# Kernel tuning notes

Measured on AMD Instinct MI355X. Metric: run time of the kernel, lower is better.

The kernel has to match this reference:

```python
import jax, jax.numpy as jnp
import numpy as np


def setup_inputs() -> dict:
    key = jax.random.key(0)
    k1, k2, k3, k4 = jax.random.split(key, 4)
    B, C, H, Wd = 32, 512, 32, 32
    sparse_dim, dict_size, feature_dim = 1024, 1024, 512
    x = jax.random.normal(k1, (B, C, H, Wd), dtype=jnp.float32)
    dictionary = jax.random.normal(k2, (dict_size, feature_dim), dtype=jnp.float32)
    # scale W, S like the LISTA init (|| . || ~ O(1)) so iterates stay bounded
    W = jax.random.normal(k3, (sparse_dim, feature_dim), dtype=jnp.float32) * 0.02
    S = jax.random.normal(k4, (sparse_dim, sparse_dim), dtype=jnp.float32) * 0.02
    thresh = jnp.float32(0.1)
    return {"x": x, "dictionary": dictionary, "W": W, "S": S, "thresh": thresh, "num_steps": 5}


def _soft_threshold(z, thresh):
    return jnp.sign(z) * jnp.maximum(jnp.abs(z) - thresh, 0.0)


def reference(x, dictionary, W, S, thresh, num_steps):
    B, C, H, Wd = x.shape
    sparse_dim = S.shape[0]
    # [B,C,H,W] -> [B*H*W, C]
    x_flat = jnp.transpose(x, (0, 2, 3, 1)).reshape(-1, C)
    dict_norm = dictionary / jnp.linalg.norm(dictionary, axis=1, keepdims=True)
    # W @ x^T is loop-invariant; compute once. [K, N]
    Wx = W @ x_flat.T
    z = jnp.zeros((sparse_dim, x_flat.shape[0]), dtype=x.dtype)
    for _ in range(num_steps):
        z = z + Wx
        z = z - S @ z
        z = _soft_threshold(z, thresh)
    # [K,N] -> [B,K,H,W]
    z = jnp.transpose(z.T.reshape(B, H, Wd, sparse_dim), (0, 3, 1, 2))
    return (z, dict_norm)
```

## Files before the change

### kernel.cpp

```cpp
#include <hip/hip_runtime.h>
#include <hip/hip_bf16.h>

typedef __bf16 bf16_t;
typedef __bf16 bf16x4 __attribute__((ext_vector_type(4)));
typedef __bf16 bf16x8 __attribute__((ext_vector_type(8)));
typedef float f32x4 __attribute__((ext_vector_type(4)));

#define GLOAD_LDS16(g, l)                                                      \
  __builtin_amdgcn_global_load_lds(                                            \
      (const __attribute__((address_space(1))) void*)(g),                      \
      (__attribute__((address_space(3))) void*)(l), 16, 0, 0)

#define MFMA(a, b, c) __builtin_amdgcn_mfma_f32_16x16x32_bf16((a), (b), (c), 0, 0, 0)

__global__ __launch_bounds__(512, 2) void gemm_kernel(
    const bf16_t* __restrict__ A, const bf16_t* __restrict__ Bt,
    int Kd, int Nc, int mode,
    const bf16_t* __restrict__ WxIn, bf16_t* __restrict__ UnextOrWx,
    float* __restrict__ Out, const float* __restrict__ thresh_p)
{
  __shared__ __align__(16) char smem[147456];
  bf16_t* lds = (bf16_t*)smem;

  const int tid = threadIdx.x;
  const int wid = tid >> 6, lane = tid & 63;
  const int wr = wid >> 1, wc = wid & 1;
  const int lr = lane & 15, kg = lane >> 4;

  const int per = gridDim.x >> 3;
  const int logical = (blockIdx.x & 7) * per + (blockIdx.x >> 3);
  const int ntn = Nc >> 7;
  const int tileN = (logical % ntn) << 7;
  const int tileM = (logical / ntn) << 8;
  const int NT = Kd >> 6;

  size_t offA[4]; int dstA[4];
  #pragma unroll
  for (int j = 0; j < 4; ++j) {
    const int f = j * 512 + tid;
    const int row = f >> 3, u = f & 7;
    const int ug = u ^ (row & 7);
    offA[j] = (size_t)(tileM + row) * Kd + ug * 8;
    dstA[j] = f * 8;
  }
  size_t offB[2]; int dstB[2];
  #pragma unroll
  for (int j = 0; j < 2; ++j) {
    const int f = j * 512 + tid;
    const int col = f >> 3, u = f & 7;
    const int ug = u ^ (col & 7);
    offB[j] = (size_t)(tileN + col) * Kd + ug * 8;
    dstB[j] = 16384 + f * 8;
  }

  auto readA = [&](int mi, int ks, int bs) -> bf16x8 {
    const int R = wr * 64 + mi * 16 + lr;
    const int ul = (ks * 4 + kg) ^ (R & 7);
    return *(const bf16x8*)(lds + bs + R * 64 + ul * 8);
  };
  auto readB = [&](int ni, int ks, int bs) -> bf16x8 {
    const int C = wc * 64 + ni * 16 + lr;
    const int ul = (ks * 4 + kg) ^ (C & 7);
    return *(const bf16x8*)(lds + bs + 16384 + C * 64 + ul * 8);
  };

  f32x4 acc[4][4] = {};
  bf16x8 a0[4], b0[4], a1[4], b1[4];

  #pragma unroll
  for (int j = 0; j < 4; ++j) GLOAD_LDS16(A + offA[j], lds + dstA[j]);
  #pragma unroll
  for (int j = 0; j < 2; ++j) GLOAD_LDS16(Bt + offB[j], lds + dstB[j]);
  if (NT > 1) {
    #pragma unroll
    for (int j = 0; j < 4; ++j) GLOAD_LDS16(A + offA[j] + 64, lds + 24576 + dstA[j]);
    #pragma unroll
    for (int j = 0; j < 2; ++j) GLOAD_LDS16(Bt + offB[j] + 64, lds + 24576 + dstB[j]);
  }
  asm volatile("s_waitcnt vmcnt(6)" ::: "memory");
  __builtin_amdgcn_s_barrier();

  int buf = 0, sb3 = 2;
  for (int t = 0; t < NT; ++t) {
    const int bs = buf * 24576;
    const int sbs = sb3 * 24576;
    const int ts = (t + 2 < NT) ? t + 2 : t + 2 - NT;
    const size_t ko = (size_t)ts << 6;

    GLOAD_LDS16(A + offA[0] + ko, lds + sbs + dstA[0]);
    GLOAD_LDS16(A + offA[1] + ko, lds + sbs + dstA[1]);
    GLOAD_LDS16(A + offA[2] + ko, lds + sbs + dstA[2]);
    GLOAD_LDS16(A + offA[3] + ko, lds + sbs + dstA[3]);
    GLOAD_LDS16(Bt + offB[0] + ko, lds + sbs + dstB[0]);
    GLOAD_LDS16(Bt + offB[1] + ko, lds + sbs + dstB[1]);

    #pragma unroll
    for (int mi = 0; mi < 4; ++mi) a0[mi] = readA(mi, 0, bs);
    #pragma unroll
    for (int ni = 0; ni < 4; ++ni) b0[ni] = readB(ni, 0, bs);
    #pragma unroll
    for (int mi = 0; mi < 4; ++mi) a1[mi] = readA(mi, 1, bs);
    #pragma unroll
    for (int ni = 0; ni < 4; ++ni) b1[ni] = readB(ni, 1, bs);

    #pragma unroll
    for (int mi = 0; mi < 4; ++mi)
      #pragma unroll
      for (int ni = 0; ni < 4; ++ni)
        acc[mi][ni] = MFMA(a0[mi], b0[ni], acc[mi][ni]);
    #pragma unroll
    for (int mi = 0; mi < 4; ++mi)
      #pragma unroll
      for (int ni = 0; ni < 4; ++ni)
        acc[mi][ni] = MFMA(a1[mi], b1[ni], acc[mi][ni]);

    asm volatile("s_waitcnt vmcnt(6)" ::: "memory");
    __builtin_amdgcn_s_barrier();

    buf = (buf == 2) ? 0 : buf + 1;
    sb3 = (sb3 == 2) ? 0 : sb3 + 1;
  }

  const float th = *thresh_p;

  if (mode <= 1) {
    asm volatile("s_waitcnt vmcnt(0)" ::: "memory");
    __syncthreads();
    float* Tl = (float*)smem;
    #pragma unroll
    for (int c = 0; c < 8; ++c) {
      if (c) __syncthreads();
      if (wr == (c >> 1)) {
        #pragma unroll
        for (int mj = 0; mj < 2; ++mj) {
          const int mi = (c & 1) * 2 + mj;
          const int rl = mj * 16 + kg * 4;
          #pragma unroll
          for (int ni = 0; ni < 4; ++ni) {
            const int cl = wc * 64 + ni * 16 + lr;
            #pragma unroll
            for (int r = 0; r < 4; ++r)
              Tl[(rl + r) * 132 + cl] = acc[mi][ni][r];
          }
        }
      }
      __syncthreads();
      #pragma unroll
      for (int j = 0; j < 2; ++j) {
        const int f  = j * 512 + tid;
        const int rl = f >> 5;
        const int c4 = (f & 31) * 4;
        const f32x4 v = *(const f32x4*)&Tl[rl * 132 + c4];
        const int grow = tileM + c * 32 + rl;
        const size_t gidx = (size_t)grow * Nc + tileN + c4;
        bf16x4 ov;
        if (mode == 1) {
          const bf16x4 wx = *(const bf16x4*)&WxIn[gidx];
          #pragma unroll
          for (int e = 0; e < 4; ++e) {
            const float a  = fabsf(v[e]) - th;
            const float zn = (a > 0.f) ? copysignf(a, v[e]) : 0.f;
            ov[e] = (bf16_t)(zn + (float)wx[e]);
          }
        } else {
          #pragma unroll
          for (int e = 0; e < 4; ++e) ov[e] = (bf16_t)v[e];
        }
        *(bf16x4*)&UnextOrWx[gidx] = ov;
      }
    }
  } else {
    #pragma unroll
    for (int mi = 0; mi < 4; ++mi)
      #pragma unroll
      for (int ni = 0; ni < 4; ++ni)
        #pragma unroll
        for (int r = 0; r < 4; ++r) {
          const float v = acc[mi][ni][r];
          const float a = fabsf(v) - th;
          acc[mi][ni][r] = (a > 0.f) ? copysignf(a, v) : 0.f;
        }
    asm volatile("s_waitcnt vmcnt(0)" ::: "memory");
    __syncthreads();
    float* Tl = (float*)smem;
    const int    bb    = tileM >> 10;
    const size_t obase = (size_t)bb * 1048576 + (size_t)(tileM & 1023);
    #pragma unroll
    for (int ch = 0; ch < 4; ++ch) {
      if (ch) __syncthreads();
      if (wc == (ch >> 1)) {
        #pragma unroll
        for (int nj = 0; nj < 2; ++nj) {
          const int ni = (ch & 1) * 2 + nj;
          const int cp = nj * 16 + lr;
          #pragma unroll
          for (int mi = 0; mi < 4; ++mi)
            #pragma unroll
            for (int r = 0; r < 4; ++r)
              Tl[cp * 260 + wr * 64 + mi * 16 + kg * 4 + r] = acc[mi][ni][r];
        }
      }
      __syncthreads();
      #pragma unroll
      for (int j = 0; j < 4; ++j) {
        const int f  = j * 512 + tid;
        const int cp = f >> 6;
        const int p4 = (f & 63) * 4;
        const f32x4 v = *(const f32x4*)&Tl[cp * 260 + p4];
        *(f32x4*)&Out[obase + (size_t)(tileN + ch * 32 + cp) * 1024 + p4] = v;
      }
    }
  }
}

__global__ __launch_bounds__(512, 2) void gemm_dual_kernel(
    const bf16_t* __restrict__ A, const bf16_t* __restrict__ B1,
    const bf16_t* __restrict__ B2,
    bf16_t* __restrict__ WxOut, bf16_t* __restrict__ UOut,
    const float* __restrict__ thresh_p)
{
  __shared__ __align__(16) char smem[131072];
  bf16_t* lds = (bf16_t*)smem;

  const int tid = threadIdx.x;
  const int wid = tid >> 6, lane = tid & 63;
  const int wr = wid >> 1, wc = wid & 1;
  const int lr = lane & 15, kg = lane >> 4;

  const int per = gridDim.x >> 3;
  const int logical = (blockIdx.x & 7) * per + (blockIdx.x >> 3);
  const int tileN = (logical & 7) << 7;
  const int tileM = (logical >> 3) << 8;

  size_t offA[4]; int dstA[4];
  #pragma unroll
  for (int j = 0; j < 4; ++j) {
    const int f = j * 512 + tid;
    const int row = f >> 3, u = f & 7;
    const int ug = u ^ (row & 7);
    offA[j] = (size_t)(tileM + row) * 512 + ug * 8;
    dstA[j] = f * 8;
  }
  size_t offB[2]; int dstB1[2], dstB2[2];
  #pragma unroll
  for (int j = 0; j < 2; ++j) {
    const int f = j * 512 + tid;
    const int col = f >> 3, u = f & 7;
    const int ug = u ^ (col & 7);
    offB[j] = (size_t)(tileN + col) * 512 + ug * 8;
    dstB1[j] = 16384 + f * 8;
    dstB2[j] = 24576 + f * 8;
  }

  auto readA = [&](int mi, int ks, int bs) -> bf16x8 {
    const int R = wr * 64 + mi * 16 + lr;
    const int ul = (ks * 4 + kg) ^ (R & 7);
    return *(const bf16x8*)(lds + bs + R * 64 + ul * 8);
  };
  auto readB = [&](int boff, int ni, int ks, int bs) -> bf16x8 {
    const int C = wc * 64 + ni * 16 + lr;
    const int ul = (ks * 4 + kg) ^ (C & 7);
    return *(const bf16x8*)(lds + bs + boff + C * 64 + ul * 8);
  };

  f32x4 accW[4][4] = {}, accT[4][4] = {};
  bf16x8 af[4], bw[4], bt[4];

  auto stageTile = [&](int ts, int sbs) {
    const size_t ko = (size_t)ts << 6;
    #pragma unroll
    for (int j = 0; j < 4; ++j) GLOAD_LDS16(A + offA[j] + ko, lds + sbs + dstA[j]);
    #pragma unroll
    for (int j = 0; j < 2; ++j) GLOAD_LDS16(B1 + offB[j] + ko, lds + sbs + dstB1[j]);
    #pragma unroll
    for (int j = 0; j < 2; ++j) GLOAD_LDS16(B2 + offB[j] + ko, lds + sbs + dstB2[j]);
  };

  stageTile(0, 0);
  asm volatile("s_waitcnt vmcnt(0)" ::: "memory");
  __builtin_amdgcn_s_barrier();

  for (int t = 0; t < 8; ++t) {
    const int bs  = (t & 1) << 15;
    const int sbs = bs ^ 32768;
    stageTile((t + 1 < 8) ? t + 1 : 0, sbs);

    #pragma unroll
    for (int ks = 0; ks < 2; ++ks) {
      #pragma unroll
      for (int mi = 0; mi < 4; ++mi) af[mi] = readA(mi, ks, bs);
      #pragma unroll
      for (int ni = 0; ni < 4; ++ni) bw[ni] = readB(16384, ni, ks, bs);
      #pragma unroll
      for (int ni = 0; ni < 4; ++ni) bt[ni] = readB(24576, ni, ks, bs);
      #pragma unroll
      for (int mi = 0; mi < 4; ++mi)
        #pragma unroll
        for (int ni = 0; ni < 4; ++ni) {
          accW[mi][ni] = MFMA(af[mi], bw[ni], accW[mi][ni]);
          accT[mi][ni] = MFMA(af[mi], bt[ni], accT[mi][ni]);
        }
    }

    asm volatile("s_waitcnt vmcnt(0)" ::: "memory");
    __builtin_amdgcn_s_barrier();
  }

  const float th = *thresh_p;
  asm volatile("s_waitcnt vmcnt(0)" ::: "memory");
  __syncthreads();
  float* Tl = (float*)smem;

  #pragma unroll
  for (int c = 0; c < 8; ++c) {
    if (c) __syncthreads();
    if (wr == (c >> 1)) {
      #pragma unroll
      for (int mj = 0; mj < 2; ++mj) {
        const int mi = (c & 1) * 2 + mj;
        const int rl = mj * 16 + kg * 4;
        #pragma unroll
        for (int ni = 0; ni < 4; ++ni) {
          const int cl = wc * 64 + ni * 16 + lr;
          #pragma unroll
          for (int r = 0; r < 4; ++r)
            Tl[(rl + r) * 132 + cl] = accW[mi][ni][r];
        }
      }
    }
    __syncthreads();
    f32x4 vw[2];
    #pragma unroll
    for (int j = 0; j < 2; ++j) {
      const int f  = j * 512 + tid;
      const int rl = f >> 5;
      const int c4 = (f & 31) * 4;
      vw[j] = *(const f32x4*)&Tl[rl * 132 + c4];
      const int grow = tileM + c * 32 + rl;
      const size_t gidx = (size_t)grow * 1024 + tileN + c4;
      bf16x4 ov;
      #pragma unroll
      for (int e = 0; e < 4; ++e) ov[e] = (bf16_t)vw[j][e];
      *(bf16x4*)&WxOut[gidx] = ov;
    }
    __syncthreads();
    if (wr == (c >> 1)) {
      #pragma unroll
      for (int mj = 0; mj < 2; ++mj) {
        const int mi = (c & 1) * 2 + mj;
        const int rl = mj * 16 + kg * 4;
        #pragma unroll
        for (int ni = 0; ni < 4; ++ni) {
          const int cl = wc * 64 + ni * 16 + lr;
          #pragma unroll
          for (int r = 0; r < 4; ++r)
            Tl[(rl + r) * 132 + cl] = accT[mi][ni][r];
        }
      }
    }
    __syncthreads();
    #pragma unroll
    for (int j = 0; j < 2; ++j) {
      const int f  = j * 512 + tid;
      const int rl = f >> 5;
      const int c4 = (f & 31) * 4;
      const f32x4 vt = *(const f32x4*)&Tl[rl * 132 + c4];
      const int grow = tileM + c * 32 + rl;
      const size_t gidx = (size_t)grow * 1024 + tileN + c4;
      bf16x4 ov;
      #pragma unroll
      for (int e = 0; e < 4; ++e) {
        const float a  = fabsf(vt[e]) - th;
        const float zn = (a > 0.f) ? copysignf(a, vt[e]) : 0.f;
        ov[e] = (bf16_t)(zn + vw[j][e]);
      }
      *(bf16x4*)&UOut[gidx] = ov;
    }
  }
}

__global__ __launch_bounds__(256) void tw_gemm_kernel(
    const bf16_t* __restrict__ Tb,
    const bf16_t* __restrict__ Wt,
    bf16_t* __restrict__ TW)
{
  const int tid = threadIdx.x;
  const int wid = tid >> 6, lane = tid & 63;
  const int lr = lane & 15, kg = lane >> 4;
  const int tile = blockIdx.x * 4 + wid;
  const int ci = tile & 31;
  const int ii = tile >> 5;
  const int i0 = ii * 16, c0 = ci * 16;

  const bf16_t* pa = Tb + (size_t)(i0 + lr) * 1024 + kg * 8;
  const bf16_t* pb = Wt + (size_t)(c0 + lr) * 1024 + kg * 8;

  f32x4 acc = {};
  #pragma unroll 4
  for (int t = 0; t < 32; ++t) {
    const bf16x8 a = *(const bf16x8*)(pa + t * 32);
    const bf16x8 b = *(const bf16x8*)(pb + t * 32);
    acc = MFMA(a, b, acc);
  }
  #pragma unroll
  for (int r = 0; r < 4; ++r)
    TW[(size_t)(i0 + kg * 4 + r) * 512 + c0 + lr] = (bf16_t)acc[r];
}

__global__ void make_T_castW_kernel(const float* __restrict__ S,
                                    bf16_t* __restrict__ T,
                                    const float* __restrict__ W,
                                    bf16_t* __restrict__ Wb) {
  const int idx = blockIdx.x * blockDim.x + threadIdx.x;
  const int i = idx >> 10, j = idx & 1023;
  T[idx] = (bf16_t)(((i == j) ? 1.0f : 0.0f) - S[idx]);
  if (idx < 524288) Wb[idx] = (bf16_t)W[idx];
}

__global__ void transpose_cast_x_kernel(const float* __restrict__ x,
                                        bf16_t* __restrict__ xt) {
  __shared__ float t[32][33];
  const int b  = blockIdx.z;
  const int p0 = blockIdx.x * 32;
  const int c0 = blockIdx.y * 32;
  const int tx = threadIdx.x, ty = threadIdx.y;
  #pragma unroll
  for (int i = 0; i < 32; i += 8)
    t[ty + i][tx] = x[((size_t)b * 512 + c0 + ty + i) * 1024 + p0 + tx];
  __syncthreads();
  #pragma unroll
  for (int i = 0; i < 32; i += 8)
    xt[((size_t)b * 1024 + p0 + ty + i) * 512 + c0 + tx] = (bf16_t)t[tx][ty + i];
}

__global__ void transpose_cast_w_kernel(const float* __restrict__ W,
                                        bf16_t* __restrict__ Wt) {
  __shared__ float t[32][33];
  const int j0 = blockIdx.x * 32;
  const int c0 = blockIdx.y * 32;
  const int tx = threadIdx.x, ty = threadIdx.y;
  #pragma unroll
  for (int i = 0; i < 32; i += 8)
    t[ty + i][tx] = W[(size_t)(j0 + ty + i) * 512 + c0 + tx];
  __syncthreads();
  #pragma unroll
  for (int i = 0; i < 32; i += 8)
    Wt[(size_t)(c0 + ty + i) * 1024 + j0 + tx] = (bf16_t)t[tx][ty + i];
}

__global__ void dict_norm_kernel(const float* __restrict__ dict,
                                 float* __restrict__ out) {
  const int row = blockIdx.x;
  const int tid = threadIdx.x;
  const float* r = dict + (size_t)row * 512;
  float s = 0.f;
  for (int i = tid; i < 512; i += 256) { float v = r[i]; s += v * v; }
  #pragma unroll
  for (int off = 32; off > 0; off >>= 1) s += __shfl_down(s, off);
  __shared__ float ps[4];
  if ((tid & 63) == 0) ps[tid >> 6] = s;
  __syncthreads();
  const float inv = 1.0f / sqrtf(ps[0] + ps[1] + ps[2] + ps[3]);
  for (int i = tid; i < 512; i += 256) out[(size_t)row * 512 + i] = r[i] * inv;
}

extern "C" void kernel_launch(void* const* d_in, const int* in_sizes, int n_in,
                              void* d_out, int out_size, void* d_ws, size_t ws_size,
                              hipStream_t stream) {
  const float* x      = (const float*)d_in[0];
  const float* dict   = (const float*)d_in[1];
  const float* W      = (const float*)d_in[2];
  const float* S      = (const float*)d_in[3];
  const float* thresh = (const float*)d_in[4];

  float* out = (float*)d_out;

  char* ws = (char*)d_ws;
  bf16_t* uA   = (bf16_t*)ws;
  bf16_t* uB   = (bf16_t*)(ws + 67108864);
  bf16_t* WxBf = (bf16_t*)(ws + 134217728);
  bf16_t* xt   = (bf16_t*)(ws + 201326592);
  bf16_t* Wbf  = (bf16_t*)(ws + 234881024);
  bf16_t* Tbf  = (bf16_t*)(ws + 235929600);

  bf16_t* WtBf = (bf16_t*)out;
  bf16_t* TWbf = WtBf + 524288;
  float* dnorm = out + 33554432;

  make_T_castW_kernel<<<dim3(2048), dim3(512), 0, stream>>>(S, Tbf, W, Wbf);
  transpose_cast_w_kernel<<<dim3(32, 16), dim3(32, 8), 0, stream>>>(W, WtBf);
  tw_gemm_kernel<<<dim3(512), dim3(256), 0, stream>>>(Tbf, WtBf, TWbf);
  transpose_cast_x_kernel<<<dim3(32, 16, 32), dim3(32, 8), 0, stream>>>(x, xt);
  dict_norm_kernel<<<dim3(1024), dim3(256), 0, stream>>>(dict, dnorm);

  gemm_dual_kernel<<<dim3(1024), dim3(512), 0, stream>>>(
      xt, Wbf, TWbf, WxBf, uA, thresh);

  bf16_t* uc = uA; bf16_t* un = uB;
  for (int s = 0; s < 3; ++s) {
    gemm_kernel<<<dim3(1024), dim3(512), 0, stream>>>(
        uc, Tbf, 1024, 1024, 1, WxBf, un, nullptr, thresh);
    bf16_t* tmp = uc; uc = un; un = tmp;
  }
  gemm_kernel<<<dim3(1024), dim3(512), 0, stream>>>(
      uc, Tbf, 1024, 1024, 2, nullptr, nullptr, out, thresh);
}
```

Measured before the change: 504.9 us.

## Load B operand directly from global into registers, staging only A in LDS

Operand B is no longer staged in LDS. Each wave loads its B fragments straight from global memory into registers, double-buffered one k-tile ahead, while A keeps the 3-stage LDS pipeline. This cuts LDS traffic and footprint (147KB to 98KB) and removes the B LDS reads. The cost is redundant global loads of B across the waves that share a column, plus more registers. The wait count was raised to account for the extra outstanding loads, which looks fragile, and the unroll by two assumes NT is even.

```diff
diff --git a/kernel.cpp b/kernel.cpp
--- a/kernel.cpp
+++ b/kernel.cpp
@@ -19,7 +19,7 @@
     const bf16_t* __restrict__ WxIn, bf16_t* __restrict__ UnextOrWx,
     float* __restrict__ Out, const float* __restrict__ thresh_p)
 {
-  __shared__ __align__(16) char smem[147456];
+  __shared__ __align__(16) char smem[98304];
   bf16_t* lds = (bf16_t*)smem;
 
   const int tid = threadIdx.x;
@@ -43,82 +43,78 @@
     offA[j] = (size_t)(tileM + row) * Kd + ug * 8;
     dstA[j] = f * 8;
   }
-  size_t offB[2]; int dstB[2];
-  #pragma unroll
-  for (int j = 0; j < 2; ++j) {
-    const int f = j * 512 + tid;
-    const int col = f >> 3, u = f & 7;
-    const int ug = u ^ (col & 7);
-    offB[j] = (size_t)(tileN + col) * Kd + ug * 8;
-    dstB[j] = 16384 + f * 8;
-  }
+
+  const bf16_t* baseB = Bt + (size_t)(tileN + wc * 64 + lr) * Kd + kg * 8;
+  const size_t strideB16 = (size_t)16 * Kd;
 
   auto readA = [&](int mi, int ks, int bs) -> bf16x8 {
     const int R = wr * 64 + mi * 16 + lr;
     const int ul = (ks * 4 + kg) ^ (R & 7);
     return *(const bf16x8*)(lds + bs + R * 64 + ul * 8);
   };
-  auto readB = [&](int ni, int ks, int bs) -> bf16x8 {
-    const int C = wc * 64 + ni * 16 + lr;
-    const int ul = (ks * 4 + kg) ^ (C & 7);
-    return *(const bf16x8*)(lds + bs + 16384 + C * 64 + ul * 8);
-  };
 
   f32x4 acc[4][4] = {};
-  bf16x8 a0[4], b0[4], a1[4], b1[4];
-
-  #pragma unroll
-  for (int j = 0; j < 4; ++j) GLOAD_LDS16(A + offA[j], lds + dstA[j]);
-  #pragma unroll
-  for (int j = 0; j < 2; ++j) GLOAD_LDS16(Bt + offB[j], lds + dstB[j]);
-  if (NT > 1) {
-    #pragma unroll
-    for (int j = 0; j < 4; ++j) GLOAD_LDS16(A + offA[j] + 64, lds + 24576 + dstA[j]);
-    #pragma unroll
-    for (int j = 0; j < 2; ++j) GLOAD_LDS16(Bt + offB[j] + 64, lds + 24576 + dstB[j]);
-  }
-  asm volatile("s_waitcnt vmcnt(6)" ::: "memory");
-  __builtin_amdgcn_s_barrier();
+  bf16x8 a0[4], a1[4];
+  bf16x8 bA[8], bB[8];
 
   int buf = 0, sb3 = 2;
-  for (int t = 0; t < NT; ++t) {
-    const int bs = buf * 24576;
-    const int sbs = sb3 * 24576;
+
+  auto iter = [&](int t, bf16x8 (&bc)[8], bf16x8 (&bn)[8]) {
+    const int bs = buf * 16384;
+    const int sbs = sb3 * 16384;
+    const int tb = (t + 1 < NT) ? t + 1 : 0;
     const int ts = (t + 2 < NT) ? t + 2 : t + 2 - NT;
+    const size_t kb = (size_t)tb << 6;
     const size_t ko = (size_t)ts << 6;
 
+    #pragma unroll
+    for (int ni = 0; ni < 4; ++ni) {
+      bn[ni]     = *(const bf16x8*)(baseB + ni * strideB16 + kb);
+      bn[ni + 4] = *(const bf16x8*)(baseB + ni * strideB16 + kb + 32);
+    }
     GLOAD_LDS16(A + offA[0] + ko, lds + sbs + dstA[0]);
     GLOAD_LDS16(A + offA[1] + ko, lds + sbs + dstA[1]);
     GLOAD_LDS16(A + offA[2] + ko, lds + sbs + dstA[2]);
     GLOAD_LDS16(A + offA[3] + ko, lds + sbs + dstA[3]);
-    GLOAD_LDS16(Bt + offB[0] + ko, lds + sbs + dstB[0]);
-    GLOAD_LDS16(Bt + offB[1] + ko, lds + sbs + dstB[1]);
 
     #pragma unroll
     for (int mi = 0; mi < 4; ++mi) a0[mi] = readA(mi, 0, bs);
     #pragma unroll
-    for (int ni = 0; ni < 4; ++ni) b0[ni] = readB(ni, 0, bs);
-    #pragma unroll
     for (int mi = 0; mi < 4; ++mi) a1[mi] = readA(mi, 1, bs);
-    #pragma unroll
-    for (int ni = 0; ni < 4; ++ni) b1[ni] = readB(ni, 1, bs);
 
     #pragma unroll
     for (int mi = 0; mi < 4; ++mi)
       #pragma unroll
       for (int ni = 0; ni < 4; ++ni)
-        acc[mi][ni] = MFMA(a0[mi], b0[ni], acc[mi][ni]);
+        acc[mi][ni] = MFMA(a0[mi], bc[ni], acc[mi][ni]);
     #pragma unroll
     for (int mi = 0; mi < 4; ++mi)
       #pragma unroll
       for (int ni = 0; ni < 4; ++ni)
-        acc[mi][ni] = MFMA(a1[mi], b1[ni], acc[mi][ni]);
-
-    asm volatile("s_waitcnt vmcnt(6)" ::: "memory");
+        acc[mi][ni] = MFMA(a1[mi], bc[ni + 4], acc[mi][ni]);
+
+    asm volatile("s_waitcnt vmcnt(12)" ::: "memory");
     __builtin_amdgcn_s_barrier();
 
     buf = (buf == 2) ? 0 : buf + 1;
     sb3 = (sb3 == 2) ? 0 : sb3 + 1;
+  };
+
+  #pragma unroll
+  for (int j = 0; j < 4; ++j) GLOAD_LDS16(A + offA[j], lds + dstA[j]);
+  #pragma unroll
+  for (int j = 0; j < 4; ++j) GLOAD_LDS16(A + offA[j] + 64, lds + 16384 + dstA[j]);
+  #pragma unroll
+  for (int ni = 0; ni < 4; ++ni) {
+    bA[ni]     = *(const bf16x8*)(baseB + ni * strideB16);
+    bA[ni + 4] = *(const bf16x8*)(baseB + ni * strideB16 + 32);
+  }
+  asm volatile("s_waitcnt vmcnt(12)" ::: "memory");
+  __builtin_amdgcn_s_barrier();
+
+  for (int t = 0; t < NT; t += 2) {
+    iter(t,     bA, bB);
+    iter(t + 1, bB, bA);
   }
 
   const float th = *thresh_p;
```

Result: slower. 862.6 us (+70.9%).

## Use 256x256 tiles with 8-wave phased ping-pong pipeline in iteration GEMMs

Applied to the files above, without the earlier changes.

Replaces the 256x128 triple-buffered GEMM with a 256x256 tile kernel (8 waves in a 2x4 grid, 128x64 per wave) and a double-buffered LDS schedule. Each K-step is split into four quadrant phases that interleave LDS reads, async global-to-LDS staging and MFMA bursts, with barriers and s_setprio around the MFMA sections. The larger tile raises arithmetic intensity and halves the grid to 512 blocks. The costs are more accumulator registers, a K dimension hardcoded to 1024, and many more barriers per step.

```diff
diff --git a/kernel.cpp b/kernel.cpp
--- a/kernel.cpp
+++ b/kernel.cpp
@@ -13,112 +13,156 @@
 
 #define MFMA(a, b, c) __builtin_amdgcn_mfma_f32_16x16x32_bf16((a), (b), (c), 0, 0, 0)
 
-__global__ __launch_bounds__(512, 2) void gemm_kernel(
+__global__ __launch_bounds__(512, 2) void gemm8_kernel(
     const bf16_t* __restrict__ A, const bf16_t* __restrict__ Bt,
-    int Kd, int Nc, int mode,
+    int Nc, int mode,
     const bf16_t* __restrict__ WxIn, bf16_t* __restrict__ UnextOrWx,
     float* __restrict__ Out, const float* __restrict__ thresh_p)
 {
-  __shared__ __align__(16) char smem[147456];
+  __shared__ __align__(16) char smem[131072];
   bf16_t* lds = (bf16_t*)smem;
 
   const int tid = threadIdx.x;
   const int wid = tid >> 6, lane = tid & 63;
-  const int wr = wid >> 1, wc = wid & 1;
+  const int wr = wid >> 2, wc = wid & 3;
   const int lr = lane & 15, kg = lane >> 4;
 
   const int per = gridDim.x >> 3;
   const int logical = (blockIdx.x & 7) * per + (blockIdx.x >> 3);
-  const int ntn = Nc >> 7;
-  const int tileN = (logical % ntn) << 7;
+  const int ntn = Nc >> 8;
+  const int tileN = (logical % ntn) << 8;
   const int tileM = (logical / ntn) << 8;
-  const int NT = Kd >> 6;
-
-  size_t offA[4]; int dstA[4];
-  #pragma unroll
-  for (int j = 0; j < 4; ++j) {
-    const int f = j * 512 + tid;
-    const int row = f >> 3, u = f & 7;
-    const int ug = u ^ (row & 7);
-    offA[j] = (size_t)(tileM + row) * Kd + ug * 8;
-    dstA[j] = f * 8;
-  }
-  size_t offB[2]; int dstB[2];
-  #pragma unroll
-  for (int j = 0; j < 2; ++j) {
-    const int f = j * 512 + tid;
-    const int col = f >> 3, u = f & 7;
-    const int ug = u ^ (col & 7);
-    offB[j] = (size_t)(tileN + col) * Kd + ug * 8;
-    dstB[j] = 16384 + f * 8;
-  }
-
-  auto readA = [&](int mi, int ks, int bs) -> bf16x8 {
-    const int R = wr * 64 + mi * 16 + lr;
+
+  const int f1 = tid + 512;
+  const int rowS[2] = { tid >> 3, f1 >> 3 };
+  const int ugS[2]  = { (tid & 7) ^ (rowS[0] & 7), (f1 & 7) ^ (rowS[1] & 7) };
+  const int dstS[2] = { tid * 8, f1 * 8 };
+
+  auto stageA = [&](int h, int kt, int slot) {
+    #pragma unroll
+    for (int j = 0; j < 2; ++j)
+      GLOAD_LDS16(A + (size_t)(tileM + h * 128 + rowS[j]) * 1024 + (kt << 6) + ugS[j] * 8,
+                  lds + slot * 32768 + h * 8192 + dstS[j]);
+  };
+  auto stageB = [&](int h, int kt, int slot) {
+    #pragma unroll
+    for (int j = 0; j < 2; ++j)
+      GLOAD_LDS16(Bt + (size_t)(tileN + h * 128 + rowS[j]) * 1024 + (kt << 6) + ugS[j] * 8,
+                  lds + slot * 32768 + 16384 + h * 8192 + dstS[j]);
+  };
+  auto readA = [&](int mi, int ks, int slot) -> bf16x8 {
+    const int R = wr * 128 + mi * 16 + lr;
     const int ul = (ks * 4 + kg) ^ (R & 7);
-    return *(const bf16x8*)(lds + bs + R * 64 + ul * 8);
-  };
-  auto readB = [&](int ni, int ks, int bs) -> bf16x8 {
+    return *(const bf16x8*)(lds + slot * 32768 + R * 64 + ul * 8);
+  };
+  auto readB = [&](int ni, int ks, int slot) -> bf16x8 {
     const int C = wc * 64 + ni * 16 + lr;
     const int ul = (ks * 4 + kg) ^ (C & 7);
-    return *(const bf16x8*)(lds + bs + 16384 + C * 64 + ul * 8);
-  };
-
-  f32x4 acc[4][4] = {};
-  bf16x8 a0[4], b0[4], a1[4], b1[4];
-
-  #pragma unroll
-  for (int j = 0; j < 4; ++j) GLOAD_LDS16(A + offA[j], lds + dstA[j]);
-  #pragma unroll
-  for (int j = 0; j < 2; ++j) GLOAD_LDS16(Bt + offB[j], lds + dstB[j]);
-  if (NT > 1) {
-    #pragma unroll
-    for (int j = 0; j < 4; ++j) GLOAD_LDS16(A + offA[j] + 64, lds + 24576 + dstA[j]);
-    #pragma unroll
-    for (int j = 0; j < 2; ++j) GLOAD_LDS16(Bt + offB[j] + 64, lds + 24576 + dstB[j]);
-  }
-  asm volatile("s_waitcnt vmcnt(6)" ::: "memory");
+    return *(const bf16x8*)(lds + slot * 32768 + 16384 + C * 64 + ul * 8);
+  };
+
+  f32x4 acc[8][4] = {};
+  bf16x8 aL[4][2], aH[4][2], bL[2][2], bH[2][2];
+
+  auto loadALo = [&](int s) {
+    #pragma unroll
+    for (int mi = 0; mi < 4; ++mi) { aL[mi][0] = readA(mi, 0, s); aL[mi][1] = readA(mi, 1, s); }
+  };
+  auto loadAHi = [&](int s) {
+    #pragma unroll
+    for (int mi = 0; mi < 4; ++mi) { aH[mi][0] = readA(mi + 4, 0, s); aH[mi][1] = readA(mi + 4, 1, s); }
+  };
+  auto loadBLo = [&](int s) {
+    #pragma unroll
+    for (int ni = 0; ni < 2; ++ni) { bL[ni][0] = readB(ni, 0, s); bL[ni][1] = readB(ni, 1, s); }
+  };
+  auto loadBHi = [&](int s) {
+    #pragma unroll
+    for (int ni = 0; ni < 2; ++ni) { bH[ni][0] = readB(ni + 2, 0, s); bH[ni][1] = readB(ni + 2, 1, s); }
+  };
+  auto q00 = [&]() {
+    #pragma unroll
+    for (int mi = 0; mi < 4; ++mi)
+      #pragma unroll
+      for (int ni = 0; ni < 2; ++ni) {
+        acc[mi][ni] = MFMA(aL[mi][0], bL[ni][0], acc[mi][ni]);
+        acc[mi][ni] = MFMA(aL[mi][1], bL[ni][1], acc[mi][ni]);
+      }
+  };
+  auto q01 = [&]() {
+    #pragma unroll
+    for (int mi = 0; mi < 4; ++mi)
+      #pragma unroll
+      for (int ni = 0; ni < 2; ++ni) {
+        acc[mi][ni + 2] = MFMA(aL[mi][0], bH[ni][0], acc[mi][ni + 2]);
+        acc[mi][ni + 2] = MFMA(aL[mi][1], bH[ni][1], acc[mi][ni + 2]);
+      }
+  };
+  auto q11 = [&]() {
+    #pragma unroll
+    for (int mi = 0; mi < 4; ++mi)
+      #pragma unroll
+      for (int ni = 0; ni < 2; ++ni) {
+        acc[mi + 4][ni + 2] = MFMA(aH[mi][0], bH[ni][0], acc[mi + 4][ni + 2]);
+        acc[mi + 4][ni + 2] = MFMA(aH[mi][1], bH[ni][1], acc[mi + 4][ni + 2]);
+      }
+  };
+  auto q10 = [&]() {
+    #pragma unroll
+    for (int mi = 0; mi < 4; ++mi)
+      #pragma unroll
+      for (int ni = 0; ni < 2; ++ni) {
+        acc[mi + 4][ni] = MFMA(aH[mi][0], bL[ni][0], acc[mi + 4][ni]);
+        acc[mi + 4][ni] = MFMA(aH[mi][1], bL[ni][1], acc[mi + 4][ni]);
+      }
+  };
+
+#define PH_SYNC()                                                              \
+  do {                                                                         \
+    __builtin_amdgcn_s_barrier();                                              \
+    asm volatile("s_waitcnt lgkmcnt(0)" ::: "memory");                         \
+    __builtin_amdgcn_sched_barrier(0);                                         \
+    __builtin_amdgcn_s_setprio(1);                                             \
+  } while (0)
+#define PH_END()                                                               \
+  do {                                                                         \
+    __builtin_amdgcn_s_setprio(0);                                             \
+    __builtin_amdgcn_s_barrier();                                              \
+  } while (0)
+#define PH_END_VM()                                                            \
+  do {                                                                         \
+    __builtin_amdgcn_s_setprio(0);                                             \
+    asm volatile("s_waitcnt vmcnt(4)" ::: "memory");                           \
+    __builtin_amdgcn_s_barrier();                                              \
+  } while (0)
+
+  stageB(0, 0, 0); stageB(1, 0, 0); stageA(0, 0, 0); stageA(1, 0, 0);
+  stageB(0, 1, 1); stageB(1, 1, 1);
+  asm volatile("s_waitcnt vmcnt(4)" ::: "memory");
   __builtin_amdgcn_s_barrier();
 
-  int buf = 0, sb3 = 2;
-  for (int t = 0; t < NT; ++t) {
-    const int bs = buf * 24576;
-    const int sbs = sb3 * 24576;
-    const int ts = (t + 2 < NT) ? t + 2 : t + 2 - NT;
-    const size_t ko = (size_t)ts << 6;
-
-    GLOAD_LDS16(A + offA[0] + ko, lds + sbs + dstA[0]);
-    GLOAD_LDS16(A + offA[1] + ko, lds + sbs + dstA[1]);
-    GLOAD_LDS16(A + offA[2] + ko, lds + sbs + dstA[2]);
-    GLOAD_LDS16(A + offA[3] + ko, lds + sbs + dstA[3]);
-    GLOAD_LDS16(Bt + offB[0] + ko, lds + sbs + dstB[0]);
-    GLOAD_LDS16(Bt + offB[1] + ko, lds + sbs + dstB[1]);
-
-    #pragma unroll
-    for (int mi = 0; mi < 4; ++mi) a0[mi] = readA(mi, 0, bs);
-    #pragma unroll
-    for (int ni = 0; ni < 4; ++ni) b0[ni] = readB(ni, 0, bs);
-    #pragma unroll
-    for (int mi = 0; mi < 4; ++mi) a1[mi] = readA(mi, 1, bs);
-    #pragma unroll
-    for (int ni = 0; ni < 4; ++ni) b1[ni] = readB(ni, 1, bs);
-
-    #pragma unroll
-    for (int mi = 0; mi < 4; ++mi)
-      #pragma unroll
-      for (int ni = 0; ni < 4; ++ni)
-        acc[mi][ni] = MFMA(a0[mi], b0[ni], acc[mi][ni]);
-    #pragma unroll
-    for (int mi = 0; mi < 4; ++mi)
-      #pragma unroll
-      for (int ni = 0; ni < 4; ++ni)
-        acc[mi][ni] = MFMA(a1[mi], b1[ni], acc[mi][ni]);
-
-    asm volatile("s_waitcnt vmcnt(6)" ::: "memory");
-    __builtin_amdgcn_s_barrier();
-
-    buf = (buf == 2) ? 0 : buf + 1;
-    sb3 = (sb3 == 2) ? 0 : sb3 + 1;
+  for (int it = 0; it < 8; ++it) {
+    const int t1 = 2 * it + 1;
+    const int n0 = (2 * it + 2) & 15;
+    const int n1 = (2 * it + 3) & 15;
+
+    loadALo(0); loadBLo(0); stageA(0, t1, 1);
+    PH_SYNC(); q00(); PH_END();
+    loadBHi(0);             stageA(1, t1, 1);
+    PH_SYNC(); q01(); PH_END();
+    loadAHi(0);             stageB(0, n0, 0);
+    PH_SYNC(); q11(); PH_END();
+                            stageB(1, n0, 0);
+    PH_SYNC(); q10(); PH_END_VM();
+
+    loadALo(1); loadBLo(1); stageA(0, n0, 0);
+    PH_SYNC(); q00(); PH_END();
+    loadBHi(1);             stageA(1, n0, 0);
+    PH_SYNC(); q01(); PH_END();
+    loadAHi(1);             stageB(0, n1, 1);
+    PH_SYNC(); q11(); PH_END();
+                            stageB(1, n1, 1);
+    PH_SYNC(); q10(); PH_END_VM();
   }
 
   const float th = *thresh_p;
@@ -130,27 +174,27 @@
     #pragma unroll
     for (int c = 0; c < 8; ++c) {
       if (c) __syncthreads();
-      if (wr == (c >> 1)) {
+      if (wr == (c >> 2)) {
         #pragma unroll
         for (int mj = 0; mj < 2; ++mj) {
-          const int mi = (c & 1) * 2 + mj;
+          const int mi = (c & 3) * 2 + mj;
           const int rl = mj * 16 + kg * 4;
           #pragma unroll
           for (int ni = 0; ni < 4; ++ni) {
             const int cl = wc * 64 + ni * 16 + lr;
             #pragma unroll
             for (int r = 0; r < 4; ++r)
-              Tl[(rl + r) * 132 + cl] = acc[mi][ni][r];
+              Tl[(rl + r) * 260 + cl] = acc[mi][ni][r];
           }
         }
       }
       __syncthreads();
       #pragma unroll
-      for (int j = 0; j < 2; ++j) {
+      for (int j = 0; j < 4; ++j) {
         const int f  = j * 512 + tid;
-        const int rl = f >> 5;
-        const int c4 = (f & 31) * 4;
-        const f32x4 v = *(const f32x4*)&Tl[rl * 132 + c4];
+        const int rl = f >> 6;
+        const int c4 = (f & 63) * 4;
+        const f32x4 v = *(const f32x4*)&Tl[rl * 260 + c4];
         const int grow = tileM + c * 32 + rl;
         const size_t gidx = (size_t)grow * Nc + tileN + c4;
         bf16x4 ov;
@@ -171,7 +215,7 @@
     }
   } else {
     #pragma unroll
-    for (int mi = 0; mi < 4; ++mi)
+    for (int mi = 0; mi < 8; ++mi)
       #pragma unroll
       for (int ni = 0; ni < 4; ++ni)
         #pragma unroll
@@ -186,7 +230,7 @@
     const int    bb    = tileM >> 10;
     const size_t obase = (size_t)bb * 1048576 + (size_t)(tileM & 1023);
     #pragma unroll
-    for (int ch = 0; ch < 4; ++ch) {
+    for (int ch = 0; ch < 8; ++ch) {
       if (ch) __syncthreads();
       if (wc == (ch >> 1)) {
         #pragma unroll
@@ -194,10 +238,10 @@
           const int ni = (ch & 1) * 2 + nj;
           const int cp = nj * 16 + lr;
           #pragma unroll
-          for (int mi = 0; mi < 4; ++mi)
+          for (int mi = 0; mi < 8; ++mi)
             #pragma unroll
             for (int r = 0; r < 4; ++r)
-              Tl[cp * 260 + wr * 64 + mi * 16 + kg * 4 + r] = acc[mi][ni][r];
+              Tl[cp * 260 + wr * 128 + mi * 16 + kg * 4 + r] = acc[mi][ni][r];
         }
       }
       __syncthreads();
@@ -211,6 +255,9 @@
       }
     }
   }
+#undef PH_SYNC
+#undef PH_END
+#undef PH_END_VM
 }
 
 __global__ __launch_bounds__(512, 2) void gemm_dual_kernel(
@@ -498,10 +545,10 @@
 
   bf16_t* uc = uA; bf16_t* un = uB;
   for (int s = 0; s < 3; ++s) {
-    gemm_kernel<<<dim3(1024), dim3(512), 0, stream>>>(
-        uc, Tbf, 1024, 1024, 1, WxBf, un, nullptr, thresh);
+    gemm8_kernel<<<dim3(512), dim3(512), 0, stream>>>(
+        uc, Tbf, 1024, 1, WxBf, un, nullptr, thresh);
     bf16_t* tmp = uc; uc = un; un = tmp;
   }
-  gemm_kernel<<<dim3(1024), dim3(512), 0, stream>>>(
-      uc, Tbf, 1024, 1024, 2, nullptr, nullptr, out, thresh);
-}
+  gemm8_kernel<<<dim3(512), dim3(512), 0, stream>>>(
+      uc, Tbf, 1024, 2, nullptr, nullptr, out, thresh);
+}
```

Measured after the change: 532.9 us. +5.6%, slower.
